# Kernel optimization log

Measured on AMD Instinct MI355X. Metric: run time of the kernel, lower is better.

## Reference

```python
import jax, jax.numpy as jnp
import numpy as np

B, T, D, L, N_MELS, MAX_R = 128, 1024, 256, 512, 80, 20

def setup_inputs() -> dict:
    key = jax.random.key(0)
    ks = jax.random.split(key, 40)
    s = 0.05
    inp = {
        'encoder_seq': jax.random.normal(ks[0], (B, T, D), jnp.float32),
        'encoder_seq_proj': jax.random.normal(ks[1], (B, T, D), jnp.float32),
        'prenet_in': jax.random.normal(ks[2], (B, N_MELS), jnp.float32),
        'attn_hidden': jax.random.normal(ks[3], (B, D), jnp.float32),
        'rnn1_hidden': jax.random.normal(ks[4], (B, L), jnp.float32),
        'rnn2_hidden': jax.random.normal(ks[5], (B, L), jnp.float32),
        'rnn1_cell': jax.random.normal(ks[6], (B, L), jnp.float32),
        'rnn2_cell': jax.random.normal(ks[7], (B, L), jnp.float32),
        'context_vec': jax.random.normal(ks[8], (B, D), jnp.float32),
        # PreNet
        'fc1_W': jax.random.normal(ks[9], (256, N_MELS), jnp.float32) * s,
        'fc1_b': jnp.zeros((256,), jnp.float32),
        'fc2_W': jax.random.normal(ks[10], (128, 256), jnp.float32) * s,
        'fc2_b': jnp.zeros((128,), jnp.float32),
        # Attention
        'attn_W': jax.random.normal(ks[11], (D, D), jnp.float32) * s,
        'attn_v': jax.random.normal(ks[12], (1, D), jnp.float32) * s,
        # GRUCell: input size D + D//2 = 384
        'gru_Wih': jax.random.normal(ks[13], (3 * D, D + D // 2), jnp.float32) * s,
        'gru_Whh': jax.random.normal(ks[14], (3 * D, D), jnp.float32) * s,
        'gru_bih': jnp.zeros((3 * D,), jnp.float32),
        'gru_bhh': jnp.zeros((3 * D,), jnp.float32),
        # rnn_input Linear: 2*D -> L
        'rnn_in_W': jax.random.normal(ks[15], (L, 2 * D), jnp.float32) * s,
        'rnn_in_b': jnp.zeros((L,), jnp.float32),
        # LSTMCell 1
        'l1_Wih': jax.random.normal(ks[16], (4 * L, L), jnp.float32) * s,
        'l1_Whh': jax.random.normal(ks[17], (4 * L, L), jnp.float32) * s,
        'l1_bih': jnp.zeros((4 * L,), jnp.float32),
        'l1_bhh': jnp.zeros((4 * L,), jnp.float32),
        # LSTMCell 2
        'l2_Wih': jax.random.normal(ks[18], (4 * L, L), jnp.float32) * s,
        'l2_Whh': jax.random.normal(ks[19], (4 * L, L), jnp.float32) * s,
        'l2_bih': jnp.zeros((4 * L,), jnp.float32),
        'l2_bhh': jnp.zeros((4 * L,), jnp.float32),
        # mel projection (no bias)
        'mel_W': jax.random.normal(ks[20], (N_MELS * MAX_R, L), jnp.float32) * s,
        'r': 2,
    }
    return inp


def _lstm_cell(x, h, c, Wih, Whh, bih, bhh):
    g = x @ Wih.T + bih + h @ Whh.T + bhh
    i, f, gg, o = jnp.split(g, 4, axis=-1)
    c_new = jax.nn.sigmoid(f) * c + jax.nn.sigmoid(i) * jnp.tanh(gg)
    h_new = jax.nn.sigmoid(o) * jnp.tanh(c_new)
    return h_new, c_new


def reference(encoder_seq, encoder_seq_proj, prenet_in, attn_hidden, rnn1_hidden,
              rnn2_hidden, rnn1_cell, rnn2_cell, context_vec,
              fc1_W, fc1_b, fc2_W, fc2_b, attn_W, attn_v,
              gru_Wih, gru_Whh, gru_bih, gru_bhh, rnn_in_W, rnn_in_b,
              l1_Wih, l1_Whh, l1_bih, l1_bhh, l2_Wih, l2_Whh, l2_bih, l2_bhh,
              mel_W, r):
    # PreNet (eval mode: dropout identity)
    p = jax.nn.relu(prenet_in @ fc1_W.T + fc1_b)
    p = jax.nn.relu(p @ fc2_W.T + fc2_b)  # [B, D//2]

    # GRUCell (torch semantics)
    x_in = jnp.concatenate([context_vec, p], axis=-1)  # [B, D + D//2]
    gi = x_in @ gru_Wih.T + gru_bih
    gh = attn_hidden @ gru_Whh.T + gru_bhh
    i_r, i_z, i_n = jnp.split(gi, 3, axis=-1)
    h_r, h_z, h_n = jnp.split(gh, 3, axis=-1)
    rg = jax.nn.sigmoid(i_r + h_r)
    zg = jax.nn.sigmoid(i_z + h_z)
    ng = jnp.tanh(i_n + rg * h_n)
    attn_h = (1.0 - zg) * ng + zg * attn_hidden  # [B, D]

    # Bahdanau attention, softmax over time (dim=1)
    q = attn_h @ attn_W.T  # [B, D]
    u = jnp.tanh(encoder_seq_proj + q[:, None, :]) @ attn_v.T  # [B, T, 1]
    scores = jax.nn.softmax(u, axis=1)
    scores_t = jnp.swapaxes(scores, 1, 2)  # [B, 1, T]
    context = jnp.matmul(scores_t, encoder_seq)[:, 0, :]  # [B, D]

    x = jnp.concatenate([context, attn_h], axis=1) @ rnn_in_W.T + rnn_in_b  # [B, L]

    rnn1_h, rnn1_c = _lstm_cell(x, rnn1_hidden, rnn1_cell, l1_Wih, l1_Whh, l1_bih, l1_bhh)
    x = x + rnn1_h
    rnn2_h, rnn2_c = _lstm_cell(x, rnn2_hidden, rnn2_cell, l2_Wih, l2_Whh, l2_bih, l2_bhh)
    x = x + rnn2_h

    mels = (x @ mel_W.T).reshape(x.shape[0], N_MELS, MAX_R)[:, :, :r]
    return (mels, scores_t, attn_h, rnn1_h, rnn2_h, rnn1_c, rnn2_c, context)
```

## Files before the change

### kernel.cpp

```cpp
#include <hip/hip_runtime.h>
#include <math.h>

#define B_   128
#define T_   1024
#define D_   256
#define L_   512

__device__ __forceinline__ float sigmoidf_(float x) {
    return 1.f / (1.f + __expf(-x));
}
__device__ __forceinline__ float tanhf_(float x) {
    x = fminf(fmaxf(x, -15.f), 15.f);
    float e = __expf(2.f * x);
    return (e - 1.f) / (e + 1.f);
}
__device__ __forceinline__ float tanh_fast(float x) {
    float e = __expf(2.f * x);
    return 1.f - 2.f * __builtin_amdgcn_rcpf(e + 1.f);
}
__device__ __forceinline__ float waveReduceSum(float v) {
    #pragma unroll
    for (int o = 32; o > 0; o >>= 1) v += __shfl_xor(v, o, 64);
    return v;
}

__global__ __launch_bounds__(256) void k1a_prenet(
    const float* __restrict__ prenet_in,
    const float* __restrict__ fc1_W, const float* __restrict__ fc1_b,
    const float* __restrict__ fc2_W, const float* __restrict__ fc2_b,
    float* __restrict__ p2_out)
{
    const int b = blockIdx.x, t = threadIdx.x;
    __shared__ __align__(16) float pin[80];
    __shared__ __align__(16) float p1[256];

    if (t < 80) pin[t] = prenet_in[b * 80 + t];
    __syncthreads();

    {
        float a = fc1_b[t];
        const float4* w  = (const float4*)(fc1_W + t * 80);
        const float4* xv = (const float4*)pin;
        #pragma unroll
        for (int k = 0; k < 20; k++) {
            float4 wv = w[k], v = xv[k];
            a += v.x * wv.x + v.y * wv.y + v.z * wv.z + v.w * wv.w;
        }
        p1[t] = fmaxf(a, 0.f);
    }
    __syncthreads();

    if (t < 128) {
        float a = fc2_b[t];
        const float4* w  = (const float4*)(fc2_W + t * 256);
        const float4* xv = (const float4*)p1;
        #pragma unroll 8
        for (int k = 0; k < 64; k++) {
            float4 wv = w[k], v = xv[k];
            a += v.x * wv.x + v.y * wv.y + v.z * wv.z + v.w * wv.w;
        }
        p2_out[b * 128 + t] = fmaxf(a, 0.f);
    }
}

__global__ __launch_bounds__(256) void k1b_gru_gemv(
    const float* __restrict__ context_vec, const float* __restrict__ p2,
    const float* __restrict__ attn_hidden,
    const float* __restrict__ gru_Wih, const float* __restrict__ gru_Whh,
    const float* __restrict__ gru_bih, const float* __restrict__ gru_bhh,
    float* __restrict__ gi_out, float* __restrict__ gh_out)
{
    const int t = threadIdx.x;
    const int j = blockIdx.x * 256 + t;
    const int b0 = blockIdx.y * 2;

    __shared__ __align__(16) float xs[2][384];
    __shared__ __align__(16) float hs[2][256];

    for (int i = t; i < 768; i += 256) {
        int bb = i / 384, k = i % 384;
        xs[bb][k] = (k < 256) ? context_vec[(b0 + bb) * 256 + k]
                              : p2[(b0 + bb) * 128 + (k - 256)];
    }
    for (int i = t; i < 512; i += 256) {
        hs[i / 256][i % 256] = attn_hidden[(b0 + i / 256) * 256 + (i % 256)];
    }
    __syncthreads();

    {
        float a0 = gru_bih[j], a1 = a0;
        const float4* w  = (const float4*)(gru_Wih + (size_t)j * 384);
        const float4* x0 = (const float4*)xs[0];
        const float4* x1 = (const float4*)xs[1];
        #pragma unroll 8
        for (int k = 0; k < 96; k++) {
            float4 wv = w[k], v0 = x0[k], v1 = x1[k];
            a0 += v0.x * wv.x + v0.y * wv.y + v0.z * wv.z + v0.w * wv.w;
            a1 += v1.x * wv.x + v1.y * wv.y + v1.z * wv.z + v1.w * wv.w;
        }
        gi_out[(size_t)(b0 + 0) * 768 + j] = a0;
        gi_out[(size_t)(b0 + 1) * 768 + j] = a1;
    }
    {
        float a0 = gru_bhh[j], a1 = a0;
        const float4* w  = (const float4*)(gru_Whh + (size_t)j * 256);
        const float4* x0 = (const float4*)hs[0];
        const float4* x1 = (const float4*)hs[1];
        #pragma unroll 8
        for (int k = 0; k < 64; k++) {
            float4 wv = w[k], v0 = x0[k], v1 = x1[k];
            a0 += v0.x * wv.x + v0.y * wv.y + v0.z * wv.z + v0.w * wv.w;
            a1 += v1.x * wv.x + v1.y * wv.y + v1.z * wv.z + v1.w * wv.w;
        }
        gh_out[(size_t)(b0 + 0) * 768 + j] = a0;
        gh_out[(size_t)(b0 + 1) * 768 + j] = a1;
    }
}

__global__ __launch_bounds__(256) void k1c_gates_q(
    const float* __restrict__ gi, const float* __restrict__ gh,
    const float* __restrict__ attn_hidden, const float* __restrict__ attn_W,
    float* __restrict__ attn_h_out, float* __restrict__ q_out)
{
    const int b = blockIdx.x, t = threadIdx.x;
    __shared__ __align__(16) float ahn[256];

    {
        float hp = attn_hidden[b * 256 + t];
        float rg = sigmoidf_(gi[(size_t)b * 768 + t]       + gh[(size_t)b * 768 + t]);
        float zg = sigmoidf_(gi[(size_t)b * 768 + 256 + t] + gh[(size_t)b * 768 + 256 + t]);
        float ng = tanhf_(gi[(size_t)b * 768 + 512 + t] + rg * gh[(size_t)b * 768 + 512 + t]);
        float h  = (1.f - zg) * ng + zg * hp;
        ahn[t] = h;
        attn_h_out[b * 256 + t] = h;
    }
    __syncthreads();

    {
        float a = 0.f;
        const float4* w  = (const float4*)(attn_W + (size_t)t * 256);
        const float4* xv = (const float4*)ahn;
        #pragma unroll 8
        for (int k = 0; k < 64; k++) {
            float4 wv = w[k], v = xv[k];
            a += v.x * wv.x + v.y * wv.y + v.z * wv.z + v.w * wv.w;
        }
        q_out[b * 256 + t] = a;
    }
}

__global__ __launch_bounds__(256, 4) void ka_attn(
    const float* __restrict__ enc_proj, const float* __restrict__ enc,
    const float* __restrict__ q, const float* __restrict__ v,
    float* __restrict__ u_out, float* __restrict__ ctx_part,
    float* __restrict__ s_part)
{
    const int b     = blockIdx.x >> 4;
    const int chunk = blockIdx.x & 15;
    const int tid   = threadIdx.x;
    const int lane  = tid & 63;
    const int wv    = tid >> 6;
    const int g     = lane >> 4;
    const int gl    = lane & 15;

    __shared__ __align__(16) float4 red[4][16][4];
    __shared__ float sred[4];

    const int t0 = chunk * 64;

    float4 qv[4], vv[4];
    #pragma unroll
    for (int c = 0; c < 4; c++) {
        qv[c] = ((const float4*)(q + b * 256))[c * 16 + gl];
        vv[c] = ((const float4*)v)[c * 16 + gl];
    }

    float4 acc[4];
    #pragma unroll
    for (int c = 0; c < 4; c++) acc[c] = make_float4(0.f, 0.f, 0.f, 0.f);
    float s_acc = 0.f;

    const float* pbase = enc_proj + ((size_t)(b * T_ + t0)) * 256;
    const float* ebase = enc      + ((size_t)(b * T_ + t0)) * 256;

    #pragma unroll
    for (int pass = 0; pass < 4; pass++) {
        const int t = wv * 16 + pass * 4 + g;
        const float4* prow = (const float4*)(pbase + (size_t)t * 256);
        const float4* erow = (const float4*)(ebase + (size_t)t * 256);

        float s = 0.f;
        #pragma unroll
        for (int c = 0; c < 4; c++) {
            float4 pj = prow[c * 16 + gl];
            s += tanh_fast(pj.x + qv[c].x) * vv[c].x
               + tanh_fast(pj.y + qv[c].y) * vv[c].y
               + tanh_fast(pj.z + qv[c].z) * vv[c].z
               + tanh_fast(pj.w + qv[c].w) * vv[c].w;
        }
        s += __shfl_xor(s, 1, 64);
        s += __shfl_xor(s, 2, 64);
        s += __shfl_xor(s, 4, 64);
        s += __shfl_xor(s, 8, 64);
        if (gl == 0) u_out[b * T_ + t0 + t] = s;

        float e = __expf(s);
        s_acc += e;
        #pragma unroll
        for (int c = 0; c < 4; c++) {
            float4 ev = erow[c * 16 + gl];
            acc[c].x += e * ev.x; acc[c].y += e * ev.y;
            acc[c].z += e * ev.z; acc[c].w += e * ev.w;
        }
    }

    #pragma unroll
    for (int c = 0; c < 4; c++) {
        acc[c].x += __shfl_xor(acc[c].x, 16, 64);
        acc[c].y += __shfl_xor(acc[c].y, 16, 64);
        acc[c].z += __shfl_xor(acc[c].z, 16, 64);
        acc[c].w += __shfl_xor(acc[c].w, 16, 64);
        acc[c].x += __shfl_xor(acc[c].x, 32, 64);
        acc[c].y += __shfl_xor(acc[c].y, 32, 64);
        acc[c].z += __shfl_xor(acc[c].z, 32, 64);
        acc[c].w += __shfl_xor(acc[c].w, 32, 64);
    }
    s_acc += __shfl_xor(s_acc, 16, 64);
    s_acc += __shfl_xor(s_acc, 32, 64);

    if (lane < 16) {
        #pragma unroll
        for (int c = 0; c < 4; c++) red[wv][gl][c] = acc[c];
    }
    if (lane == 0) sred[wv] = s_acc;
    __syncthreads();

    if (tid < 64) {
        const int c = tid >> 4, gg = tid & 15;
        float4 a0 = red[0][gg][c], a1 = red[1][gg][c];
        float4 a2 = red[2][gg][c], a3 = red[3][gg][c];
        float4 s;
        s.x = a0.x + a1.x + a2.x + a3.x;
        s.y = a0.y + a1.y + a2.y + a3.y;
        s.z = a0.z + a1.z + a2.z + a3.z;
        s.w = a0.w + a1.w + a2.w + a3.w;
        ((float4*)ctx_part)[(size_t)(b * 16 + chunk) * 64 + c * 16 + gg] = s;
    }
    if (tid == 0)
        s_part[b * 16 + chunk] = sred[0] + sred[1] + sred[2] + sred[3];
}

__global__ __launch_bounds__(256) void kb_combine(
    const float* __restrict__ u, const float* __restrict__ s_part,
    const float* __restrict__ ctx_part, const float* __restrict__ attn_h,
    float* __restrict__ scores_out, float* __restrict__ ctx_out,
    float* __restrict__ concat1)
{
    const int b = blockIdx.x, tid = threadIdx.x;
    __shared__ float ssh[16];
    if (tid < 16) ssh[tid] = s_part[b * 16 + tid];
    __syncthreads();

    float S = 0.f;
    #pragma unroll
    for (int c = 0; c < 16; c++) S += ssh[c];
    float invS = 1.f / S;

    {
        float a = 0.f;
        #pragma unroll
        for (int c = 0; c < 16; c++)
            a += ctx_part[(size_t)(b * 16 + c) * 256 + tid];
        a *= invS;
        ctx_out[b * 256 + tid] = a;
        concat1[b * 512 + tid] = a;
        concat1[b * 512 + 256 + tid] = attn_h[b * 256 + tid];
    }

    #pragma unroll
    for (int i = 0; i < 4; i++) {
        int t = i * 256 + tid;
        scores_out[b * T_ + t] = __expf(u[b * T_ + t]) * invS;
    }
}

__global__ __launch_bounds__(256) void gemm512_splitk(
    const float* __restrict__ A1, const float* __restrict__ W1,
    const float* __restrict__ A2, const float* __restrict__ W2,
    float* __restrict__ part, int N, int ksPerSeg)
{
    const int n0 = blockIdx.x * 64, m0 = blockIdx.y * 64;
    const int seg = blockIdx.z / ksPerSeg, ls = blockIdx.z % ksPerSeg;
    const int KSZ = 512 / ksPerSeg;
    const float* A = seg ? A2 : A1;
    const float* W = seg ? W2 : W1;
    const int k0 = ls * KSZ;

    __shared__ __align__(16) float As[32][68];
    __shared__ __align__(16) float Ws[32][68];

    const int tid = threadIdx.x;
    const int tm = tid & 15, tn = tid >> 4;
    const int rs = tid >> 3, qs = tid & 7;

    float acc[4][4] = {};

    for (int kt = 0; kt < KSZ; kt += 32) {
        #pragma unroll
        for (int it = 0; it < 2; it++) {
            int r = rs + it * 32;
            float4 av = *(const float4*)(A + (size_t)(m0 + r) * 512 + k0 + kt + qs * 4);
            As[qs * 4 + 0][r] = av.x; As[qs * 4 + 1][r] = av.y;
            As[qs * 4 + 2][r] = av.z; As[qs * 4 + 3][r] = av.w;
            float4 wv = *(const float4*)(W + (size_t)(n0 + r) * 512 + k0 + kt + qs * 4);
            Ws[qs * 4 + 0][r] = wv.x; Ws[qs * 4 + 1][r] = wv.y;
            Ws[qs * 4 + 2][r] = wv.z; Ws[qs * 4 + 3][r] = wv.w;
        }
        __syncthreads();
        #pragma unroll
        for (int kk = 0; kk < 32; kk++) {
            float4 a = *(const float4*)&As[kk][tm * 4];
            float4 w = *(const float4*)&Ws[kk][tn * 4];
            acc[0][0] += a.x * w.x; acc[0][1] += a.x * w.y; acc[0][2] += a.x * w.z; acc[0][3] += a.x * w.w;
            acc[1][0] += a.y * w.x; acc[1][1] += a.y * w.y; acc[1][2] += a.y * w.z; acc[1][3] += a.y * w.w;
            acc[2][0] += a.z * w.x; acc[2][1] += a.z * w.y; acc[2][2] += a.z * w.z; acc[2][3] += a.z * w.w;
            acc[3][0] += a.w * w.x; acc[3][1] += a.w * w.y; acc[3][2] += a.w * w.z; acc[3][3] += a.w * w.w;
        }
        __syncthreads();
    }

    float* pb = part + ((size_t)blockIdx.z * 128 + m0) * N + n0;
    #pragma unroll
    for (int i = 0; i < 4; i++) {
        float4 o = {acc[i][0], acc[i][1], acc[i][2], acc[i][3]};
        *(float4*)(pb + (size_t)(tm * 4 + i) * N + tn * 4) = o;
    }
}

__global__ __launch_bounds__(256) void e_rnn(
    const float* __restrict__ part, const float* __restrict__ bias,
    float* __restrict__ x)
{
    const int idx = blockIdx.x * 256 + threadIdx.x;
    const int n = idx & 511;
    float a = bias[n];
    #pragma unroll
    for (int z = 0; z < 4; z++) a += part[(size_t)z * 65536 + idx];
    x[idx] = a;
}

__global__ __launch_bounds__(256) void e_lstm(
    const float* __restrict__ part,
    const float* __restrict__ bih, const float* __restrict__ bhh,
    const float* __restrict__ c_prev, const float* __restrict__ x_prev,
    float* __restrict__ h_out, float* __restrict__ c_out, float* __restrict__ x_new)
{
    const int idx = blockIdx.x * 256 + threadIdx.x;
    const int bb = idx >> 9, j = idx & 511;
    float gi = bih[j] + bhh[j];
    float gf = bih[512 + j] + bhh[512 + j];
    float gg = bih[1024 + j] + bhh[1024 + j];
    float go = bih[1536 + j] + bhh[1536 + j];
    #pragma unroll
    for (int z = 0; z < 4; z++) {
        const float* p = part + ((size_t)z * 128 + bb) * 2048;
        gi += p[j]; gf += p[512 + j]; gg += p[1024 + j]; go += p[1536 + j];
    }
    float c = sigmoidf_(gf) * c_prev[idx] + sigmoidf_(gi) * tanhf_(gg);
    float h = sigmoidf_(go) * tanhf_(c);
    h_out[idx] = h;
    c_out[idx] = c;
    x_new[idx] = x_prev[idx] + h;
}

__global__ __launch_bounds__(512) void e_lstm2_mel(
    const float* __restrict__ part,
    const float* __restrict__ bih, const float* __restrict__ bhh,
    const float* __restrict__ c_prev, const float* __restrict__ x_prev,
    const float* __restrict__ mel_W, const int* __restrict__ r_ptr,
    float* __restrict__ h_out, float* __restrict__ c_out,
    float* __restrict__ mels)
{
    const int b = blockIdx.x, j = threadIdx.x;
    __shared__ __align__(16) float xs[512];

    const int idx = b * 512 + j;
    float gi = bih[j] + bhh[j];
    float gf = bih[512 + j] + bhh[512 + j];
    float gg = bih[1024 + j] + bhh[1024 + j];
    float go = bih[1536 + j] + bhh[1536 + j];
    #pragma unroll
    for (int z = 0; z < 4; z++) {
        const float* p = part + ((size_t)z * 128 + b) * 2048;
        gi += p[j]; gf += p[512 + j]; gg += p[1024 + j]; go += p[1536 + j];
    }
    float c = sigmoidf_(gf) * c_prev[idx] + sigmoidf_(gi) * tanhf_(gg);
    float h = sigmoidf_(go) * tanhf_(c);
    h_out[idx] = h;
    c_out[idx] = c;
    xs[j] = x_prev[idx] + h;
    __syncthreads();

    const int r = r_ptr[0];
    const int tot = 80 * r;
    for (int n = j; n < tot; n += 512) {
        int m = n / r, rr = n % r;
        const float4* w  = (const float4*)(mel_W + (size_t)(m * 20 + rr) * 512);
        const float4* xv = (const float4*)xs;
        float a = 0.f;
        #pragma unroll 8
        for (int k = 0; k < 128; k++) {
            float4 wv = w[k], vv = xv[k];
            a += wv.x * vv.x + wv.y * vv.y + wv.z * vv.z + wv.w * vv.w;
        }
        mels[(size_t)b * tot + n] = a;
    }
}

extern "C" void kernel_launch(void* const* d_in, const int* in_sizes, int n_in,
                              void* d_out, int out_size, void* d_ws, size_t ws_size,
                              hipStream_t stream)
{
    const float* enc   = (const float*)d_in[0];
    const float* encp  = (const float*)d_in[1];
    const float* pre   = (const float*)d_in[2];
    const float* ah_in = (const float*)d_in[3];
    const float* r1h   = (const float*)d_in[4];
    const float* r2h   = (const float*)d_in[5];
    const float* r1c   = (const float*)d_in[6];
    const float* r2c   = (const float*)d_in[7];
    const float* cvec  = (const float*)d_in[8];
    const float* fc1W  = (const float*)d_in[9];
    const float* fc1b  = (const float*)d_in[10];
    const float* fc2W  = (const float*)d_in[11];
    const float* fc2b  = (const float*)d_in[12];
    const float* attnW = (const float*)d_in[13];
    const float* attnv = (const float*)d_in[14];
    const float* gWih  = (const float*)d_in[15];
    const float* gWhh  = (const float*)d_in[16];
    const float* gbih  = (const float*)d_in[17];
    const float* gbhh  = (const float*)d_in[18];
    const float* rinW  = (const float*)d_in[19];
    const float* rinb  = (const float*)d_in[20];
    const float* l1Wih = (const float*)d_in[21];
    const float* l1Whh = (const float*)d_in[22];
    const float* l1bih = (const float*)d_in[23];
    const float* l1bhh = (const float*)d_in[24];
    const float* l2Wih = (const float*)d_in[25];
    const float* l2Whh = (const float*)d_in[26];
    const float* l2bih = (const float*)d_in[27];
    const float* l2bhh = (const float*)d_in[28];
    const float* melW  = (const float*)d_in[29];
    const int*   rp    = (const int*)d_in[30];

    float* out = (float*)d_out;
    float* o_mels  = out + 0;
    float* o_scor  = out + 20480;
    float* o_attnh = out + 151552;
    float* o_r1h   = out + 184320;
    float* o_r2h   = out + 249856;
    float* o_r1c   = out + 315392;
    float* o_r2c   = out + 380928;
    float* o_ctx   = out + 446464;

    float* ws     = (float*)d_ws;
    float* w_q    = ws + 0;
    float* w_u    = ws + 32768;
    float* w_s    = ws + 163840;
    float* w_ctxp = ws + 165888;
    float* w_cat1 = ws + 692224;
    float* w_x    = ws + 757760;
    float* w_x2   = ws + 823296;
    float* w_part = ws + 888832;

    float* w_p2 = w_part;
    float* w_gi = w_part + 16384;
    float* w_gh = w_part + 114688;

    hipLaunchKernelGGL(k1a_prenet, dim3(128), dim3(256), 0, stream,
                       pre, fc1W, fc1b, fc2W, fc2b, w_p2);

    hipLaunchKernelGGL(k1b_gru_gemv, dim3(3, 64), dim3(256), 0, stream,
                       cvec, w_p2, ah_in, gWih, gWhh, gbih, gbhh, w_gi, w_gh);

    hipLaunchKernelGGL(k1c_gates_q, dim3(128), dim3(256), 0, stream,
                       w_gi, w_gh, ah_in, attnW, o_attnh, w_q);

    hipLaunchKernelGGL(ka_attn, dim3(2048), dim3(256), 0, stream,
                       encp, enc, w_q, attnv, w_u, w_ctxp, w_s);

    hipLaunchKernelGGL(kb_combine, dim3(128), dim3(256), 0, stream,
                       w_u, w_s, w_ctxp, o_attnh, o_scor, o_ctx, w_cat1);

    hipLaunchKernelGGL(gemm512_splitk, dim3(8, 2, 4), dim3(256), 0, stream,
                       w_cat1, rinW, w_cat1, rinW, w_part, 512, 4);
    hipLaunchKernelGGL(e_rnn, dim3(256), dim3(256), 0, stream, w_part, rinb, w_x);

    hipLaunchKernelGGL(gemm512_splitk, dim3(32, 2, 4), dim3(256), 0, stream,
                       w_x, l1Wih, r1h, l1Whh, w_part, 2048, 2);
    hipLaunchKernelGGL(e_lstm, dim3(256), dim3(256), 0, stream,
                       w_part, l1bih, l1bhh, r1c, w_x, o_r1h, o_r1c, w_x2);

    hipLaunchKernelGGL(gemm512_splitk, dim3(32, 2, 4), dim3(256), 0, stream,
                       w_x2, l2Wih, r2h, l2Whh, w_part, 2048, 2);
    hipLaunchKernelGGL(e_lstm2_mel, dim3(128), dim3(512), 0, stream,
                       w_part, l2bih, l2bhh, r2c, w_x2, melW, rp,
                       o_r2h, o_r2c, o_mels);
}
```

Baseline: 154.8 us.

## Restructure attention kernel to one wave per block, one lane per timestep

Rewrites the attention score and context kernel to launch 64-thread blocks. Each lane computes a full 256-wide score for its own timestep, with q and v staged in LDS. The exp weights go to LDS so the context accumulation can read encoder rows coalesced, lane-per-float4. This removes the cross-wave shared-memory reduction and the shuffle reductions, but each lane now strides through separate enc_proj rows, and smaller blocks give fewer resident waves.

New measurement: 138.3 us. 1.12x faster.

```diff
diff --git a/kernel.cpp b/kernel.cpp
--- a/kernel.cpp
+++ b/kernel.cpp
@@ -149,7 +149,7 @@
     }
 }
 
-__global__ __launch_bounds__(256, 4) void ka_attn(
+__global__ __launch_bounds__(64, 2) void ka_attn(
     const float* __restrict__ enc_proj, const float* __restrict__ enc,
     const float* __restrict__ q, const float* __restrict__ v,
     float* __restrict__ u_out, float* __restrict__ ctx_part,
@@ -157,97 +157,63 @@
 {
     const int b     = blockIdx.x >> 4;
     const int chunk = blockIdx.x & 15;
-    const int tid   = threadIdx.x;
-    const int lane  = tid & 63;
-    const int wv    = tid >> 6;
-    const int g     = lane >> 4;
-    const int gl    = lane & 15;
-
-    __shared__ __align__(16) float4 red[4][16][4];
-    __shared__ float sred[4];
-
-    const int t0 = chunk * 64;
-
-    float4 qv[4], vv[4];
-    #pragma unroll
-    for (int c = 0; c < 4; c++) {
-        qv[c] = ((const float4*)(q + b * 256))[c * 16 + gl];
-        vv[c] = ((const float4*)v)[c * 16 + gl];
-    }
-
-    float4 acc[4];
-    #pragma unroll
-    for (int c = 0; c < 4; c++) acc[c] = make_float4(0.f, 0.f, 0.f, 0.f);
-    float s_acc = 0.f;
-
-    const float* pbase = enc_proj + ((size_t)(b * T_ + t0)) * 256;
-    const float* ebase = enc      + ((size_t)(b * T_ + t0)) * 256;
-
-    #pragma unroll
-    for (int pass = 0; pass < 4; pass++) {
-        const int t = wv * 16 + pass * 4 + g;
-        const float4* prow = (const float4*)(pbase + (size_t)t * 256);
-        const float4* erow = (const float4*)(ebase + (size_t)t * 256);
-
-        float s = 0.f;
-        #pragma unroll
-        for (int c = 0; c < 4; c++) {
-            float4 pj = prow[c * 16 + gl];
-            s += tanh_fast(pj.x + qv[c].x) * vv[c].x
-               + tanh_fast(pj.y + qv[c].y) * vv[c].y
-               + tanh_fast(pj.z + qv[c].z) * vv[c].z
-               + tanh_fast(pj.w + qv[c].w) * vv[c].w;
-        }
-        s += __shfl_xor(s, 1, 64);
-        s += __shfl_xor(s, 2, 64);
-        s += __shfl_xor(s, 4, 64);
-        s += __shfl_xor(s, 8, 64);
-        if (gl == 0) u_out[b * T_ + t0 + t] = s;
-
-        float e = __expf(s);
-        s_acc += e;
-        #pragma unroll
-        for (int c = 0; c < 4; c++) {
-            float4 ev = erow[c * 16 + gl];
-            acc[c].x += e * ev.x; acc[c].y += e * ev.y;
-            acc[c].z += e * ev.z; acc[c].w += e * ev.w;
-        }
-    }
-
-    #pragma unroll
-    for (int c = 0; c < 4; c++) {
-        acc[c].x += __shfl_xor(acc[c].x, 16, 64);
-        acc[c].y += __shfl_xor(acc[c].y, 16, 64);
-        acc[c].z += __shfl_xor(acc[c].z, 16, 64);
-        acc[c].w += __shfl_xor(acc[c].w, 16, 64);
-        acc[c].x += __shfl_xor(acc[c].x, 32, 64);
-        acc[c].y += __shfl_xor(acc[c].y, 32, 64);
-        acc[c].z += __shfl_xor(acc[c].z, 32, 64);
-        acc[c].w += __shfl_xor(acc[c].w, 32, 64);
-    }
-    s_acc += __shfl_xor(s_acc, 16, 64);
-    s_acc += __shfl_xor(s_acc, 32, 64);
-
-    if (lane < 16) {
-        #pragma unroll
-        for (int c = 0; c < 4; c++) red[wv][gl][c] = acc[c];
-    }
-    if (lane == 0) sred[wv] = s_acc;
-    __syncthreads();
-
-    if (tid < 64) {
-        const int c = tid >> 4, gg = tid & 15;
-        float4 a0 = red[0][gg][c], a1 = red[1][gg][c];
-        float4 a2 = red[2][gg][c], a3 = red[3][gg][c];
-        float4 s;
-        s.x = a0.x + a1.x + a2.x + a3.x;
-        s.y = a0.y + a1.y + a2.y + a3.y;
-        s.z = a0.z + a1.z + a2.z + a3.z;
-        s.w = a0.w + a1.w + a2.w + a3.w;
-        ((float4*)ctx_part)[(size_t)(b * 16 + chunk) * 64 + c * 16 + gg] = s;
-    }
-    if (tid == 0)
-        s_part[b * 16 + chunk] = sred[0] + sred[1] + sred[2] + sred[3];
+    const int lane  = threadIdx.x;
+    const int t0    = chunk * 64;
+
+    __shared__ __align__(16) float qs[256];
+    __shared__ __align__(16) float vs[256];
+    __shared__ __align__(16) float el[64];
+
+    ((float4*)qs)[lane] = ((const float4*)(q + b * 256))[lane];
+    ((float4*)vs)[lane] = ((const float4*)v)[lane];
+    __syncthreads();
+
+    const float4* prow = (const float4*)(enc_proj + ((size_t)(b * T_ + t0 + lane)) * 256);
+    const float4* qv4  = (const float4*)qs;
+    const float4* vv4  = (const float4*)vs;
+
+    float s0 = 0.f, s1 = 0.f, s2 = 0.f, s3 = 0.f;
+    #pragma unroll
+    for (int k = 0; k < 16; k += 4) {
+        float4 p0 = prow[k + 0], p1 = prow[k + 1], p2 = prow[k + 2], p3 = prow[k + 3];
+        float4 q0 = qv4[k + 0],  q1 = qv4[k + 1],  q2 = qv4[k + 2],  q3 = qv4[k + 3];
+        float4 v0 = vv4[k + 0],  v1 = vv4[k + 1],  v2 = vv4[k + 2],  v3 = vv4[k + 3];
+        s0 += tanh_fast(p0.x + q0.x) * v0.x + tanh_fast(p0.y + q0.y) * v0.y
+            + tanh_fast(p0.z + q0.z) * v0.z + tanh_fast(p0.w + q0.w) * v0.w;
+        s1 += tanh_fast(p1.x + q1.x) * v1.x + tanh_fast(p1.y + q1.y) * v1.y
+            + tanh_fast(p1.z + q1.z) * v1.z + tanh_fast(p1.w + q1.w) * v1.w;
+        s2 += tanh_fast(p2.x + q2.x) * v2.x + tanh_fast(p2.y + q2.y) * v2.y
+            + tanh_fast(p2.z + q2.z) * v2.z + tanh_fast(p2.w + q2.w) * v2.w;
+        s3 += tanh_fast(p3.x + q3.x) * v3.x + tanh_fast(p3.y + q3.y) * v3.y
+            + tanh_fast(p3.z + q3.z) * v3.z + tanh_fast(p3.w + q3.w) * v3.w;
+    }
+    float u = (s0 + s1) + (s2 + s3);
+    u_out[b * T_ + t0 + lane] = u;
+
+    float e = __expf(u);
+    el[lane] = e;
+    float ssum = waveReduceSum(e);
+    if (lane == 0) s_part[b * 16 + chunk] = ssum;
+    __syncthreads();
+
+    const float4* erow = (const float4*)(enc + ((size_t)(b * T_ + t0)) * 256);
+    const float4* e4p  = (const float4*)el;
+    float4 accA = {0.f, 0.f, 0.f, 0.f}, accB = {0.f, 0.f, 0.f, 0.f};
+
+    #pragma unroll 4
+    for (int t = 0; t < 64; t += 4) {
+        float4 e4 = e4p[t >> 2];
+        float4 r0 = erow[(size_t)(t + 0) * 64 + lane];
+        float4 r1 = erow[(size_t)(t + 1) * 64 + lane];
+        float4 r2 = erow[(size_t)(t + 2) * 64 + lane];
+        float4 r3 = erow[(size_t)(t + 3) * 64 + lane];
+        accA.x += e4.x * r0.x; accA.y += e4.x * r0.y; accA.z += e4.x * r0.z; accA.w += e4.x * r0.w;
+        accB.x += e4.y * r1.x; accB.y += e4.y * r1.y; accB.z += e4.y * r1.z; accB.w += e4.y * r1.w;
+        accA.x += e4.z * r2.x; accA.y += e4.z * r2.y; accA.z += e4.z * r2.z; accA.w += e4.z * r2.w;
+        accB.x += e4.w * r3.x; accB.y += e4.w * r3.y; accB.z += e4.w * r3.z; accB.w += e4.w * r3.w;
+    }
+    accA.x += accB.x; accA.y += accB.y; accA.z += accB.z; accA.w += accB.w;
+    ((float4*)ctx_part)[(size_t)(b * 16 + chunk) * 64 + lane] = accA;
 }
 
 __global__ __launch_bounds__(256) void kb_combine(
@@ -486,7 +452,7 @@
     hipLaunchKernelGGL(k1c_gates_q, dim3(128), dim3(256), 0, stream,
                        w_gi, w_gh, ah_in, attnW, o_attnh, w_q);
 
-    hipLaunchKernelGGL(ka_attn, dim3(2048), dim3(256), 0, stream,
+    hipLaunchKernelGGL(ka_attn, dim3(2048), dim3(64), 0, stream,
                        encp, enc, w_q, attnv, w_u, w_ctxp, w_s);
 
     hipLaunchKernelGGL(kb_combine, dim3(128), dim3(256), 0, stream,
```
